# Optimization experiments

Measured on AMD Instinct MI355X. Metric: run time of the kernel, lower is better.

The kernel has to match this reference:

```python
import jax, jax.numpy as jnp
import numpy as np

N = 100000
E = 1600000
F_IN = 128
F_OUT = 128
BN_EPS = 1e-5


def setup_inputs() -> dict:
    key = jax.random.key(0)
    ks = jax.random.split(key, 8)
    x = jax.random.normal(ks[0], (N, F_IN), dtype=jnp.float32)
    edge_index = jax.random.randint(ks[1], (2, E), 0, N, dtype=jnp.int64)
    s1 = 1.0 / np.sqrt(F_IN)
    s2 = 1.0 / np.sqrt(F_OUT)
    W1 = jax.random.uniform(ks[2], (F_OUT, F_IN), jnp.float32, -s1, s1)
    b1 = jax.random.uniform(ks[3], (F_OUT,), jnp.float32, -s1, s1)
    gamma = jnp.ones((F_OUT,), jnp.float32)
    beta = jnp.zeros((F_OUT,), jnp.float32)
    W2 = jax.random.uniform(ks[4], (F_OUT, F_OUT), jnp.float32, -s2, s2)
    b2 = jax.random.uniform(ks[5], (F_OUT,), jnp.float32, -s2, s2)
    eps = jnp.zeros((1,), jnp.float32)
    return {"x": x, "edge_index": edge_index, "eps": eps, "W1": W1, "b1": b1,
            "gamma": gamma, "beta": beta, "W2": W2, "b2": b2}


def reference(x, edge_index, eps, W1, b1, gamma, beta, W2, b2):
    row, col = edge_index[0], edge_index[1]
    # gather neighbor features then scatter-add by destination node
    neighbor_sum = jax.ops.segment_sum(x[col], row, num_segments=x.shape[0])
    out = (1.0 + eps) * x + neighbor_sum  # [N, F_IN]
    h = out @ W1.T + b1                   # [N, F_OUT]
    # BatchNorm1d in training mode: biased batch statistics over nodes
    mean = jnp.mean(h, axis=0)
    var = jnp.mean(jnp.square(h - mean), axis=0)
    h = (h - mean) * jax.lax.rsqrt(var + BN_EPS) * gamma + beta
    h = jax.nn.relu(h)
    return h @ W2.T + b2
```

## Files before the change

kernel.cpp:

```cpp
#include <hip/hip_runtime.h>
#include <hip/hip_bf16.h>

#define NF 128

typedef __attribute__((ext_vector_type(8))) short short8;
typedef __attribute__((ext_vector_type(4))) float f32x4;

__device__ __forceinline__ ushort f2bf(float f) {
    union { __hip_bfloat16 h; ushort u; } c;
    c.h = __float2bfloat16(f);
    return c.u;
}
__device__ __forceinline__ float bf_lo(uint u) { return __uint_as_float(u << 16); }
__device__ __forceinline__ float bf_hi(uint u) { return __uint_as_float(u & 0xffff0000u); }

__global__ void cvt_all_kernel(const float* __restrict__ x, const float* __restrict__ W1,
                               const float* __restrict__ W2, ushort* __restrict__ xb,
                               ushort* __restrict__ W1b, ushort* __restrict__ W2b,
                               float* __restrict__ stats, int* __restrict__ binCnt, int nx4) {
    int gid = blockIdx.x * blockDim.x + threadIdx.x;
    if (gid < 512) stats[gid] = 0.0f;
    if (gid < 256) binCnt[gid] = 0;
    const float* src;
    ushort* dst;
    int idx;
    if (gid < nx4) { src = x; dst = xb; idx = gid; }
    else if (gid < nx4 + 4096) { src = W1; dst = W1b; idx = gid - nx4; }
    else if (gid < nx4 + 8192) { src = W2; dst = W2b; idx = gid - nx4 - 4096; }
    else return;
    float4 v = reinterpret_cast<const float4*>(src)[idx];
    ushort4 o;
    o.x = f2bf(v.x); o.y = f2bf(v.y); o.z = f2bf(v.z); o.w = f2bf(v.w);
    reinterpret_cast<ushort4*>(dst)[idx] = o;
}

#define EPB 4096

__global__ void passA_kernel(const int* __restrict__ ei, int* __restrict__ blkCnt,
                             int* __restrict__ binCnt, int E) {
    __shared__ int lcnt[256];
    int t = threadIdx.x;
    lcnt[t] = 0;
    __syncthreads();
    int base = blockIdx.x * EPB;
#pragma unroll
    for (int it = 0; it < EPB / 256; it++) {
        int e = base + it * 256 + t;
        if (e < E) atomicAdd(&lcnt[ei[e] >> 9], 1);
    }
    __syncthreads();
    int c = lcnt[t];
    blkCnt[blockIdx.x * 256 + t] = c;
    if (c) atomicAdd(&binCnt[t], c);
}

__global__ void passB_kernel(const int* __restrict__ binCnt, int* __restrict__ binBase,
                             int* __restrict__ binCursor, int* __restrict__ rowptr,
                             int N, int E) {
    __shared__ int s[256];
    int t = threadIdx.x;
    int v = binCnt[t];
    s[t] = v;
    __syncthreads();
#pragma unroll
    for (int off = 1; off < 256; off <<= 1) {
        int t2 = (t >= off) ? s[t - off] : 0;
        __syncthreads();
        s[t] += t2;
        __syncthreads();
    }
    int excl = s[t] - v;
    binBase[t] = excl;
    binCursor[t] = excl;
    if (t == 0) rowptr[N] = E;
}

__global__ void passC_kernel(const int* __restrict__ ei, const int* __restrict__ blkCnt,
                             int* __restrict__ binCursor, uint2* __restrict__ pair, int E) {
    __shared__ int lbase[256];
    __shared__ int lcur[256];
    int t = threadIdx.x;
    int c = blkCnt[blockIdx.x * 256 + t];
    lbase[t] = c ? atomicAdd(&binCursor[t], c) : 0;
    lcur[t] = 0;
    __syncthreads();
    int base = blockIdx.x * EPB;
#pragma unroll
    for (int it = 0; it < EPB / 256; it++) {
        int e = base + it * 256 + t;
        if (e < E) {
            int row = ei[e];
            int col = ei[E + e];
            int b = row >> 9;
            int r = atomicAdd(&lcur[b], 1);
            pair[lbase[b] + r] = make_uint2((uint)row, (uint)col);
        }
    }
}

__global__ void passDE_kernel(const uint2* __restrict__ pair, const int* __restrict__ binBase,
                              const int* __restrict__ binCnt, int* __restrict__ rowptr,
                              int* __restrict__ adj, int N) {
    __shared__ int hist[512];
    __shared__ int s2[256];
    __shared__ int cur[512];
    int t = threadIdx.x;
    int b = blockIdx.x;
    hist[t] = 0;
    hist[t + 256] = 0;
    __syncthreads();
    int base = binBase[b], cnt = binCnt[b];
    for (int i = t; i < cnt; i += 256)
        atomicAdd(&hist[pair[base + i].x & 511], 1);
    __syncthreads();
    int h0 = hist[2 * t], h1 = hist[2 * t + 1];
    s2[t] = h0 + h1;
    __syncthreads();
#pragma unroll
    for (int off = 1; off < 256; off <<= 1) {
        int v = (t >= off) ? s2[t - off] : 0;
        __syncthreads();
        s2[t] += v;
        __syncthreads();
    }
    int e0 = base + s2[t] - (h0 + h1);
    int e1 = e0 + h0;
    int g0 = b * 512 + 2 * t;
    if (g0 < N) rowptr[g0] = e0;
    if (g0 + 1 < N) rowptr[g0 + 1] = e1;
    cur[2 * t] = e0;
    cur[2 * t + 1] = e1;
    __syncthreads();
    for (int i = t; i < cnt; i += 256) {
        uint2 p = pair[base + i];
        int slot = atomicAdd(&cur[p.x & 511], 1);
        adj[slot] = (int)p.y;
    }
}

__global__ void gather_kernel(const uint4* __restrict__ xb4, const int* __restrict__ rowptr,
                              const int* __restrict__ adj, const float* __restrict__ eps,
                              uint4* __restrict__ aggb4, int N) {
    int t = blockIdx.x * blockDim.x + threadIdx.x;
    int node = t >> 4;
    int lane = t & 15;
    if (node >= N) return;
    uint4 u = xb4[(size_t)node * 16 + lane];
    float s = 1.0f + eps[0];
    float a0 = bf_lo(u.x) * s, a1 = bf_hi(u.x) * s;
    float a2 = bf_lo(u.y) * s, a3 = bf_hi(u.y) * s;
    float a4 = bf_lo(u.z) * s, a5 = bf_hi(u.z) * s;
    float a6 = bf_lo(u.w) * s, a7 = bf_hi(u.w) * s;
    int j = rowptr[node], end = rowptr[node + 1];
    for (; j + 4 <= end; j += 4) {
        int c0 = adj[j], c1 = adj[j + 1], c2 = adj[j + 2], c3 = adj[j + 3];
        uint4 v0 = xb4[(size_t)c0 * 16 + lane];
        uint4 v1 = xb4[(size_t)c1 * 16 + lane];
        uint4 v2 = xb4[(size_t)c2 * 16 + lane];
        uint4 v3 = xb4[(size_t)c3 * 16 + lane];
        a0 += bf_lo(v0.x); a1 += bf_hi(v0.x); a2 += bf_lo(v0.y); a3 += bf_hi(v0.y);
        a4 += bf_lo(v0.z); a5 += bf_hi(v0.z); a6 += bf_lo(v0.w); a7 += bf_hi(v0.w);
        a0 += bf_lo(v1.x); a1 += bf_hi(v1.x); a2 += bf_lo(v1.y); a3 += bf_hi(v1.y);
        a4 += bf_lo(v1.z); a5 += bf_hi(v1.z); a6 += bf_lo(v1.w); a7 += bf_hi(v1.w);
        a0 += bf_lo(v2.x); a1 += bf_hi(v2.x); a2 += bf_lo(v2.y); a3 += bf_hi(v2.y);
        a4 += bf_lo(v2.z); a5 += bf_hi(v2.z); a6 += bf_lo(v2.w); a7 += bf_hi(v2.w);
        a0 += bf_lo(v3.x); a1 += bf_hi(v3.x); a2 += bf_lo(v3.y); a3 += bf_hi(v3.y);
        a4 += bf_lo(v3.z); a5 += bf_hi(v3.z); a6 += bf_lo(v3.w); a7 += bf_hi(v3.w);
    }
    for (; j < end; j++) {
        uint4 v0 = xb4[(size_t)adj[j] * 16 + lane];
        a0 += bf_lo(v0.x); a1 += bf_hi(v0.x); a2 += bf_lo(v0.y); a3 += bf_hi(v0.y);
        a4 += bf_lo(v0.z); a5 += bf_hi(v0.z); a6 += bf_lo(v0.w); a7 += bf_hi(v0.w);
    }
    uint4 o;
    o.x = (uint)f2bf(a0) | ((uint)f2bf(a1) << 16);
    o.y = (uint)f2bf(a2) | ((uint)f2bf(a3) << 16);
    o.z = (uint)f2bf(a4) | ((uint)f2bf(a5) << 16);
    o.w = (uint)f2bf(a6) | ((uint)f2bf(a7) << 16);
    aggb4[(size_t)node * 16 + lane] = o;
}

template <int MODE>
__global__ __launch_bounds__(256) void mgemm_kernel(
    const ushort* __restrict__ Ab, const ushort* __restrict__ Wb,
    const float* __restrict__ bias, float* __restrict__ out,
    ushort* __restrict__ hb, float* __restrict__ stats,
    const float* __restrict__ gamma, const float* __restrict__ beta, int N) {
    __shared__ ushort As[128 * 136];
    __shared__ ushort Bs[128 * 136];
    __shared__ float redS[256];
    __shared__ float redQ[256];
    __shared__ float scL[128];
    __shared__ float shL[128];

    const int t = threadIdx.x;
    const int row0 = blockIdx.x * 128;
    const int r16 = t >> 4;
    const int c8 = (t & 15) * 8;

    if (MODE == 1 && t < 128) {
        float inv_n = 1.0f / (float)N;
        float mean = stats[t] * inv_n;
        float var = fmaxf(stats[128 + t] * inv_n - mean * mean, 0.0f);
        float s = gamma[t] * rsqrtf(var + 1e-5f);
        scL[t] = s;
        shL[t] = beta[t] - mean * s;
    }
    if (MODE == 1) __syncthreads();

    float sc[8], sh[8];
    if (MODE == 1) {
#pragma unroll
        for (int i = 0; i < 8; i++) { sc[i] = scL[c8 + i]; sh[i] = shL[c8 + i]; }
    }

#pragma unroll
    for (int it = 0; it < 8; it++) {
        int row = it * 16 + r16;
        int gr = row0 + row;
        if (MODE == 0) {
            uint4 v = make_uint4(0, 0, 0, 0);
            if (gr < N) v = *reinterpret_cast<const uint4*>(Ab + (size_t)gr * NF + c8);
            *reinterpret_cast<uint4*>(&As[row * 136 + c8]) = v;
        } else {
            uint4 v = make_uint4(0, 0, 0, 0);
            if (gr < N) v = *reinterpret_cast<const uint4*>(hb + (size_t)gr * NF + c8);
            float vv[8] = {bf_lo(v.x), bf_hi(v.x), bf_lo(v.y), bf_hi(v.y),
                           bf_lo(v.z), bf_hi(v.z), bf_lo(v.w), bf_hi(v.w)};
#pragma unroll
            for (int i = 0; i < 8; i++) vv[i] = fmaxf(vv[i] * sc[i] + sh[i], 0.0f);
            uint4 p;
            p.x = (uint)f2bf(vv[0]) | ((uint)f2bf(vv[1]) << 16);
            p.y = (uint)f2bf(vv[2]) | ((uint)f2bf(vv[3]) << 16);
            p.z = (uint)f2bf(vv[4]) | ((uint)f2bf(vv[5]) << 16);
            p.w = (uint)f2bf(vv[6]) | ((uint)f2bf(vv[7]) << 16);
            *reinterpret_cast<uint4*>(&As[row * 136 + c8]) = p;
        }
        uint4 w = *reinterpret_cast<const uint4*>(Wb + row * NF + c8);
        *reinterpret_cast<uint4*>(&Bs[row * 136 + c8]) = w;
    }
    __syncthreads();

    const int wid = t >> 6;
    const int lane = t & 63;
    const int quad = lane >> 4;
    const int l16 = lane & 15;
    const int wm = wid >> 1;
    const int wn = wid & 1;

    f32x4 acc[4][4];
#pragma unroll
    for (int tm = 0; tm < 4; tm++)
#pragma unroll
        for (int tn = 0; tn < 4; tn++) acc[tm][tn] = (f32x4)(0.0f);

#pragma unroll
    for (int ks = 0; ks < 4; ks++) {
        short8 a[4], b[4];
#pragma unroll
        for (int tm = 0; tm < 4; tm++)
            a[tm] = *reinterpret_cast<const short8*>(
                &As[(wm * 64 + tm * 16 + l16) * 136 + ks * 32 + quad * 8]);
#pragma unroll
        for (int tn = 0; tn < 4; tn++)
            b[tn] = *reinterpret_cast<const short8*>(
                &Bs[(wn * 64 + tn * 16 + l16) * 136 + ks * 32 + quad * 8]);
#pragma unroll
        for (int tm = 0; tm < 4; tm++)
#pragma unroll
            for (int tn = 0; tn < 4; tn++)
                acc[tm][tn] = __builtin_amdgcn_mfma_f32_16x16x32_bf16(a[tm], b[tn],
                                                                      acc[tm][tn], 0, 0, 0);
    }

    float bs[4];
#pragma unroll
    for (int tn = 0; tn < 4; tn++) bs[tn] = bias[wn * 64 + tn * 16 + l16];

    float ssum[4] = {0.f, 0.f, 0.f, 0.f}, sq[4] = {0.f, 0.f, 0.f, 0.f};
#pragma unroll
    for (int tm = 0; tm < 4; tm++) {
        int rb = wm * 64 + tm * 16 + quad * 4;
#pragma unroll
        for (int reg = 0; reg < 4; reg++) {
            int gr = row0 + rb + reg;
            bool ok = gr < N;
#pragma unroll
            for (int tn = 0; tn < 4; tn++) {
                int col = wn * 64 + tn * 16 + l16;
                float h = acc[tm][tn][reg] + bs[tn];
                if (ok) {
                    if (MODE == 0) {
                        hb[(size_t)gr * NF + col] = f2bf(h);
                        ssum[tn] += h;
                        sq[tn] += h * h;
                    } else {
                        out[(size_t)gr * NF + col] = h;
                    }
                }
            }
        }
    }

    if (MODE == 0) {
#pragma unroll
        for (int tn = 0; tn < 4; tn++) {
            float s = ssum[tn], q = sq[tn];
            s += __shfl_xor(s, 16); s += __shfl_xor(s, 32);
            q += __shfl_xor(q, 16); q += __shfl_xor(q, 32);
            if (quad == 0) {
                int c = wn * 64 + tn * 16 + l16;
                redS[wm * 128 + c] = s;
                redQ[wm * 128 + c] = q;
            }
        }
        __syncthreads();
        if (t < 128) {
            unsafeAtomicAdd(&stats[t], redS[t] + redS[128 + t]);
            unsafeAtomicAdd(&stats[128 + t], redQ[t] + redQ[128 + t]);
        }
    }
}

extern "C" void kernel_launch(void* const* d_in, const int* in_sizes, int n_in,
                              void* d_out, int out_size, void* d_ws, size_t ws_size,
                              hipStream_t stream) {
    const float* x     = (const float*)d_in[0];
    const int* ei      = (const int*)d_in[1];
    const float* eps   = (const float*)d_in[2];
    const float* W1    = (const float*)d_in[3];
    const float* b1    = (const float*)d_in[4];
    const float* gamma = (const float*)d_in[5];
    const float* beta  = (const float*)d_in[6];
    const float* W2    = (const float*)d_in[7];
    const float* b2    = (const float*)d_in[8];
    float* out         = (float*)d_out;

    const int N = in_sizes[0] / NF;
    const int E = in_sizes[1] / 2;

    const int NB = (N + 511) >> 9;
    const int nblkC = (E + EPB - 1) / EPB;

    ushort* xb     = (ushort*)d_ws;
    ushort* aggb   = xb + (size_t)N * NF;
    ushort* W1b    = aggb + (size_t)N * NF;
    ushort* W2b    = W1b + NF * NF;
    float*  stats  = (float*)(W2b + NF * NF);
    int*    rowptr = (int*)(stats + 512);
    int*    binCnt = rowptr + (N + 1);
    int*    binBase   = binCnt + 256;
    int*    binCursor = binBase + 256;
    int*    blkCnt = binCursor + 256;
    int*    adj    = blkCnt + (size_t)nblkC * 256;
    uint2*  pair   = (uint2*)aggb;
    ushort* hb     = xb;

    int nx4 = N * 32;
    cvt_all_kernel<<<(nx4 + 8192 + 255) / 256, 256, 0, stream>>>(x, W1, W2, xb, W1b, W2b,
                                                                 stats, binCnt, nx4);
    passA_kernel<<<nblkC, 256, 0, stream>>>(ei, blkCnt, binCnt, E);
    passB_kernel<<<1, 256, 0, stream>>>(binCnt, binBase, binCursor, rowptr, N, E);
    passC_kernel<<<nblkC, 256, 0, stream>>>(ei, blkCnt, binCursor, pair, E);
    passDE_kernel<<<NB, 256, 0, stream>>>(pair, binBase, binCnt, rowptr, adj, N);

    long long gt = (long long)N * 16;
    gather_kernel<<<(int)((gt + 255) / 256), 256, 0, stream>>>((const uint4*)xb, rowptr, adj,
                                                               eps, (uint4*)aggb, N);

    int gblocks = (N + 127) / 128;
    mgemm_kernel<0><<<gblocks, 256, 0, stream>>>(aggb, W1b, b1, out, hb, stats,
                                                 nullptr, nullptr, N);
    mgemm_kernel<1><<<gblocks, 256, 0, stream>>>(nullptr, W2b, b2, out, hb, stats,
                                                 gamma, beta, N);
}
```

Baseline: 301.5 us.

## Fold bin scan into scatter pass and stage coalesced pair writes in LDS

Removes the single-block scan kernel and the per-block count array. The scatter pass now recounts its edges locally, computes the global bin offsets itself with a redundant 256-wide scan, and claims space through atomic per-bin offsets. It sorts pairs by bin in shared memory so global writes come out as contiguous runs. The CSR pass computes its own bin base by reduction. This saves a launch and makes writes more coalesced, at the cost of 32KB LDS per block and extra scans.

```diff
diff --git a/kernel.cpp b/kernel.cpp
--- a/kernel.cpp
+++ b/kernel.cpp
@@ -17,10 +17,11 @@
 __global__ void cvt_all_kernel(const float* __restrict__ x, const float* __restrict__ W1,
                                const float* __restrict__ W2, ushort* __restrict__ xb,
                                ushort* __restrict__ W1b, ushort* __restrict__ W2b,
-                               float* __restrict__ stats, int* __restrict__ binCnt, int nx4) {
+                               float* __restrict__ stats, int* __restrict__ binCnt,
+                               int* __restrict__ binOff, int nx4) {
     int gid = blockIdx.x * blockDim.x + threadIdx.x;
     if (gid < 512) stats[gid] = 0.0f;
-    if (gid < 256) binCnt[gid] = 0;
+    if (gid < 256) { binCnt[gid] = 0; binOff[gid] = 0; }
     const float* src;
     ushort* dst;
     int idx;
@@ -36,8 +37,7 @@
 
 #define EPB 4096
 
-__global__ void passA_kernel(const int* __restrict__ ei, int* __restrict__ blkCnt,
-                             int* __restrict__ binCnt, int E) {
+__global__ void passA_kernel(const int* __restrict__ ei, int* __restrict__ binCnt, int E) {
     __shared__ int lcnt[256];
     int t = threadIdx.x;
     lcnt[t] = 0;
@@ -50,57 +50,70 @@
     }
     __syncthreads();
     int c = lcnt[t];
-    blkCnt[blockIdx.x * 256 + t] = c;
     if (c) atomicAdd(&binCnt[t], c);
 }
 
-__global__ void passB_kernel(const int* __restrict__ binCnt, int* __restrict__ binBase,
-                             int* __restrict__ binCursor, int* __restrict__ rowptr,
-                             int N, int E) {
-    __shared__ int s[256];
+__global__ void passC_kernel(const int* __restrict__ ei, const int* __restrict__ binCnt,
+                             int* __restrict__ binOff, uint2* __restrict__ pair, int E) {
+    __shared__ uint2 sorted[EPB];
+    __shared__ int lcnt[256];
+    __shared__ int lofs[256];
+    __shared__ int scanB[256];
+    __shared__ int lcur[256];
+    __shared__ int gdelta[256];
     int t = threadIdx.x;
-    int v = binCnt[t];
-    s[t] = v;
-    __syncthreads();
-#pragma unroll
-    for (int off = 1; off < 256; off <<= 1) {
-        int t2 = (t >= off) ? s[t - off] : 0;
-        __syncthreads();
-        s[t] += t2;
-        __syncthreads();
-    }
-    int excl = s[t] - v;
-    binBase[t] = excl;
-    binCursor[t] = excl;
-    if (t == 0) rowptr[N] = E;
-}
-
-__global__ void passC_kernel(const int* __restrict__ ei, const int* __restrict__ blkCnt,
-                             int* __restrict__ binCursor, uint2* __restrict__ pair, int E) {
-    __shared__ int lbase[256];
-    __shared__ int lcur[256];
-    int t = threadIdx.x;
-    int c = blkCnt[blockIdx.x * 256 + t];
-    lbase[t] = c ? atomicAdd(&binCursor[t], c) : 0;
+    lcnt[t] = 0;
     lcur[t] = 0;
     __syncthreads();
     int base = blockIdx.x * EPB;
+    int rows[EPB / 256], cols[EPB / 256];
 #pragma unroll
     for (int it = 0; it < EPB / 256; it++) {
         int e = base + it * 256 + t;
-        if (e < E) {
-            int row = ei[e];
-            int col = ei[E + e];
-            int b = row >> 9;
-            int r = atomicAdd(&lcur[b], 1);
-            pair[lbase[b] + r] = make_uint2((uint)row, (uint)col);
-        }
-    }
-}
-
-__global__ void passDE_kernel(const uint2* __restrict__ pair, const int* __restrict__ binBase,
-                              const int* __restrict__ binCnt, int* __restrict__ rowptr,
-                              int* __restrict__ adj, int N) {
+        rows[it] = (e < E) ? ei[e] : -1;
+        cols[it] = (e < E) ? ei[E + e] : 0;
+        if (rows[it] >= 0) atomicAdd(&lcnt[rows[it] >> 9], 1);
+    }
+    __syncthreads();
+    int v = lcnt[t];
+    lofs[t] = v;
+    int bc = binCnt[t];
+    scanB[t] = bc;
+    __syncthreads();
+#pragma unroll
+    for (int off = 1; off < 256; off <<= 1) {
+        int u1 = (t >= off) ? lofs[t - off] : 0;
+        int u2 = (t >= off) ? scanB[t - off] : 0;
+        __syncthreads();
+        lofs[t] += u1;
+        scanB[t] += u2;
+        __syncthreads();
+    }
+    int myOfs = lofs[t] - v;
+    int binBase_t = scanB[t] - bc;
+    int g = v ? atomicAdd(&binOff[t], v) : 0;
+    __syncthreads();
+    lofs[t] = myOfs;
+    gdelta[t] = binBase_t + g - myOfs;
+    __syncthreads();
+#pragma unroll
+    for (int it = 0; it < EPB / 256; it++) {
+        if (rows[it] >= 0) {
+            int b = rows[it] >> 9;
+            int p = lofs[b] + atomicAdd(&lcur[b], 1);
+            sorted[p] = make_uint2((uint)rows[it], (uint)cols[it]);
+        }
+    }
+    __syncthreads();
+    int nvalid = min(EPB, E - base);
+    for (int i = t; i < nvalid; i += 256) {
+        uint2 pr = sorted[i];
+        pair[gdelta[pr.x >> 9] + i] = pr;
+    }
+}
+
+__global__ void passDE_kernel(const uint2* __restrict__ pair, const int* __restrict__ binCnt,
+                              int* __restrict__ rowptr, int* __restrict__ adj, int N, int E) {
     __shared__ int hist[512];
     __shared__ int s2[256];
     __shared__ int cur[512];
@@ -108,8 +121,16 @@
     int b = blockIdx.x;
     hist[t] = 0;
     hist[t + 256] = 0;
-    __syncthreads();
-    int base = binBase[b], cnt = binCnt[b];
+    s2[t] = (t < b) ? binCnt[t] : 0;
+    __syncthreads();
+#pragma unroll
+    for (int off = 128; off > 0; off >>= 1) {
+        if (t < off) s2[t] += s2[t + off];
+        __syncthreads();
+    }
+    int base = s2[0];
+    int cnt = binCnt[b];
+    __syncthreads();
     for (int i = t; i < cnt; i += 256)
         atomicAdd(&hist[pair[base + i].x & 511], 1);
     __syncthreads();
@@ -118,9 +139,9 @@
     __syncthreads();
 #pragma unroll
     for (int off = 1; off < 256; off <<= 1) {
-        int v = (t >= off) ? s2[t - off] : 0;
-        __syncthreads();
-        s2[t] += v;
+        int u = (t >= off) ? s2[t - off] : 0;
+        __syncthreads();
+        s2[t] += u;
         __syncthreads();
     }
     int e0 = base + s2[t] - (h0 + h1);
@@ -128,6 +149,7 @@
     int g0 = b * 512 + 2 * t;
     if (g0 < N) rowptr[g0] = e0;
     if (g0 + 1 < N) rowptr[g0 + 1] = e1;
+    if (t == 0 && b == gridDim.x - 1) rowptr[N] = E;
     cur[2 * t] = e0;
     cur[2 * t + 1] = e1;
     __syncthreads();
@@ -349,20 +371,17 @@
     float*  stats  = (float*)(W2b + NF * NF);
     int*    rowptr = (int*)(stats + 512);
     int*    binCnt = rowptr + (N + 1);
-    int*    binBase   = binCnt + 256;
-    int*    binCursor = binBase + 256;
-    int*    blkCnt = binCursor + 256;
-    int*    adj    = blkCnt + (size_t)nblkC * 256;
+    int*    binOff = binCnt + 256;
+    int*    adj    = binOff + 256;
     uint2*  pair   = (uint2*)aggb;
     ushort* hb     = xb;
 
     int nx4 = N * 32;
     cvt_all_kernel<<<(nx4 + 8192 + 255) / 256, 256, 0, stream>>>(x, W1, W2, xb, W1b, W2b,
-                                                                 stats, binCnt, nx4);
-    passA_kernel<<<nblkC, 256, 0, stream>>>(ei, blkCnt, binCnt, E);
-    passB_kernel<<<1, 256, 0, stream>>>(binCnt, binBase, binCursor, rowptr, N, E);
-    passC_kernel<<<nblkC, 256, 0, stream>>>(ei, blkCnt, binCursor, pair, E);
-    passDE_kernel<<<NB, 256, 0, stream>>>(pair, binBase, binCnt, rowptr, adj, N);
+                                                                 stats, binCnt, binOff, nx4);
+    passA_kernel<<<nblkC, 256, 0, stream>>>(ei, binCnt, E);
+    passC_kernel<<<nblkC, 256, 0, stream>>>(ei, binCnt, binOff, pair, E);
+    passDE_kernel<<<NB, 256, 0, stream>>>(pair, binCnt, rowptr, adj, N, E);
 
     long long gt = (long long)N * 16;
     gather_kernel<<<(int)((gt + 255) / 256), 256, 0, stream>>>((const uint4*)xb, rowptr, adj,
```

Measured after the change: 289.8 us. -3.9%, faster.
